# Kernel tuning notes

Measured on AMD Instinct MI355X. Metric: run time of the kernel, lower is better.

The kernel has to match this reference:

```python
import jax, jax.numpy as jnp
import numpy as np

N, E, DIN, DOUT, H = 50000, 800000, 256, 128, 8
DH = DOUT // H  # per-head dim = 16


def setup_inputs() -> dict:
    key = jax.random.key(0)
    k1, k2, k3, k4, k5 = jax.random.split(key, 5)
    x = jax.random.normal(k1, (N, DIN), dtype=jnp.float32)
    edge_index = jax.random.randint(k2, (2, E), 0, N)
    W_trans = jax.random.normal(k3, (DOUT, DIN), dtype=jnp.float32) / np.sqrt(DIN).astype(np.float32)
    W_att = jax.random.normal(k4, (1, 2 * DH), dtype=jnp.float32) / np.sqrt(2 * DH).astype(np.float32)
    b_att = jax.random.normal(k5, (1,), dtype=jnp.float32) * 0.01
    return {"x": x, "W_trans": W_trans, "W_att": W_att, "b_att": b_att, "edge_index": edge_index}


def reference(x, W_trans, W_att, b_att, edge_index):
    n = x.shape[0]
    # append self-loops (as in the torch module)
    loops = jnp.arange(n, dtype=edge_index.dtype)
    ei = jnp.concatenate([edge_index, jnp.stack([loops, loops])], axis=1)  # [2, E+N]
    src, dst = ei[0], ei[1]

    # linear transform, split heads: [n, H, DH]
    h = (x @ W_trans.T).reshape(n, H, DH)
    h_i = h[src]  # [Etot, H, DH]
    h_j = h[dst]  # [Etot, H, DH]

    # per-edge attention score: concat -> linear -> leaky_relu(0.2)
    s = jnp.concatenate([h_i, h_j], axis=-1) @ W_att.T + b_att  # [Etot, H, 1]
    s = jnp.where(s >= 0, s, 0.2 * s)

    # softmax(dim=0)*exp_sum/scatter_add(exp) == exp(s)/segment_sum(exp(s)) per dst node
    e = jnp.exp(s)
    denom = jax.ops.segment_sum(e, dst, num_segments=n)  # [n, H, 1]
    att = e / denom[dst]

    out = jax.ops.segment_sum(h_i * att, dst, num_segments=n)  # [n, H, DH]
    return out.reshape(n, DOUT)  # head_fusion='cat'
```

## Files before the change

### kernel.cpp

```cpp
#include <hip/hip_runtime.h>


constexpr int DIN  = 256;
constexpr int DOUT = 128;
constexpr int H    = 8;
constexpr int BKT  = 128;
constexpr int CAP  = 2560;
constexpr int CHUNK = 2048;
constexpr int MAXNB = 512;

typedef __attribute__((ext_vector_type(8))) short bf16x8;
typedef __attribute__((ext_vector_type(4))) float f32x4;

__device__ __forceinline__ float lrelu(float s) { return s >= 0.0f ? s : 0.2f * s; }

__device__ __forceinline__ unsigned short f2bf(float f) {
  unsigned u = __float_as_uint(f);
  u += 0x7FFF + ((u >> 16) & 1);
  return (unsigned short)(u >> 16);
}
__device__ __forceinline__ float bflo(unsigned u) { return __uint_as_float(u << 16); }
__device__ __forceinline__ float bfhi(unsigned u) { return __uint_as_float(u & 0xFFFF0000u); }

__device__ __forceinline__ int wave_incl_scan(int v, int lane) {
#pragma unroll
  for (int d = 1; d < 64; d <<= 1) {
    int t = __shfl_up(v, d, 64);
    if (lane >= d) v += t;
  }
  return v;
}

__global__ void conv_w(const float* __restrict__ W, unsigned short* __restrict__ Wbf,
                       int n, int* __restrict__ bcount, int nb) {
  int i = blockIdx.x * blockDim.x + threadIdx.x;
  if (i < n) Wbf[i] = f2bf(W[i]);
  if (i < nb) bcount[i] = 0;
}

__global__ __launch_bounds__(256) void bp(const int* __restrict__ ei,
                                          int* __restrict__ bcount,
                                          unsigned* __restrict__ pair_buf,
                                          int E, int nb) {
  __shared__ int hist[MAXNB];
  __shared__ int gbase[MAXNB];
  int c0 = blockIdx.x * CHUNK;
  for (int i = threadIdx.x; i < nb; i += 256) hist[i] = 0;
  __syncthreads();
  int dcache[8];
#pragma unroll
  for (int q = 0; q < 8; ++q) {
    int e = c0 + q * 256 + threadIdx.x;
    dcache[q] = (e < E) ? ei[E + e] : -1;
    if (dcache[q] >= 0) atomicAdd(&hist[dcache[q] >> 7], 1);
  }
  __syncthreads();
  for (int i = threadIdx.x; i < nb; i += 256) {
    int c = hist[i];
    gbase[i] = c ? atomicAdd(&bcount[i], c) : 0;
  }
  __syncthreads();
  for (int i = threadIdx.x; i < nb; i += 256) hist[i] = 0;
  __syncthreads();
  int scache[8];
#pragma unroll
  for (int q = 0; q < 8; ++q) {
    int e = c0 + q * 256 + threadIdx.x;
    scache[q] = (dcache[q] >= 0) ? ei[e] : 0;
  }
#pragma unroll
  for (int q = 0; q < 8; ++q) {
    if (dcache[q] >= 0) {
      int bk = dcache[q] >> 7;
      int r = atomicAdd(&hist[bk], 1);
      pair_buf[bk * CAP + gbase[bk] + r] =
          ((unsigned)scache[q] << 8) | (unsigned)(dcache[q] & 127);
    }
  }
}

__global__ __launch_bounds__(256, 2) void gemm(const float* __restrict__ x,
                                               const unsigned short* __restrict__ Wbf,
                                               unsigned short* __restrict__ hbf,
                                               int N) {
  __shared__ __align__(16) unsigned short Wlds[DOUT * DIN];
  {
    const int tid = threadIdx.x;
#pragma unroll
    for (int i = 0; i < 16; ++i) {
      int c = i * 256 + tid;
      int t = c >> 9, ks = (c >> 6) & 7, L = c & 63;
      const unsigned short* gp = Wbf + ((t * 16 + (L & 15)) * DIN + ks * 32 + (L >> 4) * 8);
      *(bf16x8*)&Wlds[c * 8] = *(const bf16x8*)gp;
    }
  }
  __syncthreads();
  int wid = blockIdx.x * 4 + (threadIdx.x >> 6);
  int m0 = wid * 32;
  if (m0 >= N) return;
  int lane = threadIdx.x & 63;
  int mr = lane & 15, kg = lane >> 4;
  int r0 = m0 + mr;       if (r0 >= N) r0 = N - 1;
  int r1 = m0 + 16 + mr;  if (r1 >= N) r1 = N - 1;
  const float* xr0 = x + (size_t)r0 * DIN + kg * 8;
  const float* xr1 = x + (size_t)r1 * DIN + kg * 8;
  const unsigned short* fb = Wlds + lane * 8;

  f32x4 acc[2][8];
#pragma unroll
  for (int mt = 0; mt < 2; ++mt)
#pragma unroll
    for (int t = 0; t < 8; ++t) acc[mt][t] = (f32x4){0.f, 0.f, 0.f, 0.f};

  float4 p00 = *(const float4*)xr0, p01 = *(const float4*)(xr0 + 4);
  float4 p10 = *(const float4*)xr1, p11 = *(const float4*)(xr1 + 4);
#pragma unroll
  for (int ks = 0; ks < 8; ++ks) {
    bf16x8 a0, a1;
    a0[0] = (short)f2bf(p00.x); a0[1] = (short)f2bf(p00.y);
    a0[2] = (short)f2bf(p00.z); a0[3] = (short)f2bf(p00.w);
    a0[4] = (short)f2bf(p01.x); a0[5] = (short)f2bf(p01.y);
    a0[6] = (short)f2bf(p01.z); a0[7] = (short)f2bf(p01.w);
    a1[0] = (short)f2bf(p10.x); a1[1] = (short)f2bf(p10.y);
    a1[2] = (short)f2bf(p10.z); a1[3] = (short)f2bf(p10.w);
    a1[4] = (short)f2bf(p11.x); a1[5] = (short)f2bf(p11.y);
    a1[6] = (short)f2bf(p11.z); a1[7] = (short)f2bf(p11.w);
    if (ks < 7) {
      p00 = *(const float4*)(xr0 + (ks + 1) * 32);
      p01 = *(const float4*)(xr0 + (ks + 1) * 32 + 4);
      p10 = *(const float4*)(xr1 + (ks + 1) * 32);
      p11 = *(const float4*)(xr1 + (ks + 1) * 32 + 4);
    }
#pragma unroll
    for (int t = 0; t < 8; ++t) {
      bf16x8 b = *(const bf16x8*)(fb + ((t * 8 + ks) << 9));
      acc[0][t] = __builtin_amdgcn_mfma_f32_16x16x32_bf16(a0, b, acc[0][t], 0, 0, 0);
      acc[1][t] = __builtin_amdgcn_mfma_f32_16x16x32_bf16(a1, b, acc[1][t], 0, 0, 0);
    }
  }
#pragma unroll
  for (int mt = 0; mt < 2; ++mt)
#pragma unroll
    for (int t = 0; t < 8; ++t)
#pragma unroll
      for (int r = 0; r < 4; ++r) {
        int row = m0 + mt * 16 + kg * 4 + r;
        if (row < N) hbf[(size_t)row * DOUT + t * 16 + mr] = f2bf(acc[mt][t][r]);
      }
}

__global__ __launch_bounds__(256) void node_scores(const unsigned short* __restrict__ hbf,
                                                   const float* __restrict__ Wa,
                                                   float* __restrict__ a_src,
                                                   float* __restrict__ a_dst,
                                                   int NH) {
  int idx = blockIdx.x * 256 + threadIdx.x;
  if (idx >= NH) return;
  int v = idx >> 3, hh = idx & 7;
  const unsigned short* hp = hbf + (size_t)v * DOUT + hh * 16;
  uint4 p0 = *(const uint4*)hp;
  uint4 p1 = *(const uint4*)(hp + 8);
  float hv[16];
  hv[0] = bflo(p0.x); hv[1] = bfhi(p0.x); hv[2] = bflo(p0.y); hv[3] = bfhi(p0.y);
  hv[4] = bflo(p0.z); hv[5] = bfhi(p0.z); hv[6] = bflo(p0.w); hv[7] = bfhi(p0.w);
  hv[8] = bflo(p1.x); hv[9] = bfhi(p1.x); hv[10] = bflo(p1.y); hv[11] = bfhi(p1.y);
  hv[12] = bflo(p1.z); hv[13] = bfhi(p1.z); hv[14] = bflo(p1.w); hv[15] = bfhi(p1.w);
  float s1 = 0.f, s2 = 0.f;
#pragma unroll
  for (int d = 0; d < 16; ++d) {
    s1 += hv[d] * Wa[d];
    s2 += hv[d] * Wa[16 + d];
  }
  a_src[idx] = s1;
  a_dst[idx] = s2;
}

__global__ __launch_bounds__(512) void agg(const unsigned* __restrict__ pair_buf,
                                           const int* __restrict__ bcount,
                                           const unsigned short* __restrict__ hbf,
                                           const float* __restrict__ a_src,
                                           const float* __restrict__ a_dst,
                                           const float* __restrict__ b_att,
                                           float* __restrict__ out, int N) {
  __shared__ int cnt[BKT];
  __shared__ int off[BKT];
  __shared__ int cur[BKT];
  __shared__ int wsum[2];
  __shared__ unsigned short slist[CAP];
  const int t = threadIdx.x;
  const int B = blockIdx.x;
  const int v0 = B * BKT;
  if (t < BKT) cnt[t] = 0;
  __syncthreads();
  const int cntE = min(bcount[B], CAP);
  const unsigned* reg = pair_buf + (size_t)B * CAP;
  for (int i = t; i < cntE; i += 512) atomicAdd(&cnt[reg[i] & 127], 1);
  __syncthreads();
  int val = 0, inc = 0;
  if (t < BKT) {
    val = cnt[t];
    inc = wave_incl_scan(val, t & 63);
    if ((t & 63) == 63) wsum[t >> 6] = inc;
  }
  __syncthreads();
  if (t < BKT) {
    int ex = inc - val + ((t >= 64) ? wsum[0] : 0);
    off[t] = ex;
    cur[t] = ex;
  }
  __syncthreads();
  for (int i = t; i < cntE; i += 512) {
    unsigned p = reg[i];
    int k = atomicAdd(&cur[p & 127], 1);
    slist[k] = (unsigned short)(p >> 8);
  }
  __syncthreads();
  const float bb = b_att[0];
  const int grp = t >> 4, sl = t & 15, head = sl >> 1;
  for (int nd = grp; nd < BKT; nd += 32) {
    int v = v0 + nd;
    if (v >= N) continue;
    float ad = a_dst[(size_t)v * H + head] + bb;
    int beg = off[nd], end = cur[nd];
    float a0 = 0, a1 = 0, a2 = 0, a3 = 0, a4 = 0, a5 = 0, a6 = 0, a7 = 0, den = 0;
    int sa = (beg < end) ? slist[beg] : 0;
    int sb = (beg + 1 < end) ? slist[beg + 1] : 0;
    for (int j = beg; j < end; j += 2) {
      int sa2 = (j + 2 < end) ? slist[j + 2] : 0;
      int sb2 = (j + 3 < end) ? slist[j + 3] : 0;
      float asa = a_src[(size_t)sa * H + head];
      float asb = a_src[(size_t)sb * H + head];
      uint4 ua = *(const uint4*)(hbf + (size_t)sa * DOUT + sl * 8);
      uint4 ub = *(const uint4*)(hbf + (size_t)sb * DOUT + sl * 8);
      float ea = __expf(lrelu(asa + ad));
      float eb = (j + 1 < end) ? __expf(lrelu(asb + ad)) : 0.f;
      den += ea + eb;
      a0 += ea * bflo(ua.x) + eb * bflo(ub.x);
      a1 += ea * bfhi(ua.x) + eb * bfhi(ub.x);
      a2 += ea * bflo(ua.y) + eb * bflo(ub.y);
      a3 += ea * bfhi(ua.y) + eb * bfhi(ub.y);
      a4 += ea * bflo(ua.z) + eb * bflo(ub.z);
      a5 += ea * bfhi(ua.z) + eb * bfhi(ub.z);
      a6 += ea * bflo(ua.w) + eb * bflo(ub.w);
      a7 += ea * bfhi(ua.w) + eb * bfhi(ub.w);
      sa = sa2; sb = sb2;
    }
    float es = __expf(lrelu(a_src[(size_t)v * H + head] + ad));
    uint4 u = *(const uint4*)(hbf + (size_t)v * DOUT + sl * 8);
    float inv = 1.0f / (den + es);
    float4 o0 = make_float4((a0 + es * bflo(u.x)) * inv, (a1 + es * bfhi(u.x)) * inv,
                            (a2 + es * bflo(u.y)) * inv, (a3 + es * bfhi(u.y)) * inv);
    float4 o1 = make_float4((a4 + es * bflo(u.z)) * inv, (a5 + es * bfhi(u.z)) * inv,
                            (a6 + es * bflo(u.w)) * inv, (a7 + es * bfhi(u.w)) * inv);
    *(float4*)&out[(size_t)v * DOUT + sl * 8] = o0;
    *(float4*)&out[(size_t)v * DOUT + sl * 8 + 4] = o1;
  }
}

extern "C" void kernel_launch(void* const* d_in, const int* in_sizes, int n_in,
                              void* d_out, int out_size, void* d_ws, size_t ws_size,
                              hipStream_t stream) {
  const float* x     = (const float*)d_in[0];
  const float* W     = (const float*)d_in[1];
  const float* Wa    = (const float*)d_in[2];
  const float* b_att = (const float*)d_in[3];
  const int*   ei    = (const int*)d_in[4];
  const int N  = in_sizes[0] / DIN;
  const int E  = in_sizes[4] / 2;
  const int NB = (N + BKT - 1) / BKT;
  float* out = (float*)d_out;

  char* p = (char*)d_ws;
  auto take = [&p](size_t bytes) {
    uintptr_t u = ((uintptr_t)p + 15) & ~(uintptr_t)15;
    p = (char*)(u + bytes);
    return (void*)u;
  };
  unsigned short* hbf = (unsigned short*)take((size_t)N * DOUT * 2);
  unsigned short* Wbf = (unsigned short*)take((size_t)DOUT * DIN * 2);
  float* a_src        = (float*)take((size_t)N * H * 4);
  float* a_dst        = (float*)take((size_t)N * H * 4);
  int* bcount         = (int*)take((size_t)NB * 4);
  unsigned* pair_buf  = (unsigned*)take((size_t)NB * CAP * 4);

  dim3 b256(256);
  const int cw_blocks   = (DOUT * DIN + 255) / 256;
  const int bp_blocks   = (E + CHUNK - 1) / CHUNK;
  const int gemm_blocks = ((N + 31) / 32 + 3) / 4;
  const int ns_blocks   = (N * H + 255) / 256;

  conv_w<<<dim3(cw_blocks), b256, 0, stream>>>(W, Wbf, DOUT * DIN, bcount, NB);
  bp<<<dim3(bp_blocks), b256, 0, stream>>>(ei, bcount, pair_buf, E, NB);
  gemm<<<dim3(gemm_blocks), b256, 0, stream>>>(x, Wbf, hbf, N);
  node_scores<<<dim3(ns_blocks), b256, 0, stream>>>(hbf, Wa, a_src, a_dst, N * H);
  agg<<<dim3(NB), dim3(512), 0, stream>>>(pair_buf, bcount, hbf, a_src, a_dst,
                                          b_att, out, N);
}
```

Before: 176.2 us.

## Store features head-major and split aggregation blocks per head

The transformed features and per-node scores are stored head-major ([H][N][16]). The aggregation grid is split into one block per bucket and head, with 4 lanes per destination node. Each head's gather then touches a compact 1.6 MB slice that fits better in cache, and there are eight times as many blocks for parallelism. In exchange, every block rebuilds the bucket's CSR in shared memory (eight times the pair_buf reads and LDS sorting), gathers shrink to 8-byte loads, and the GEMM writes become more scattered.

```diff
diff --git a/kernel.cpp b/kernel.cpp
--- a/kernel.cpp
+++ b/kernel.cpp
@@ -81,7 +81,7 @@
 
 __global__ __launch_bounds__(256, 2) void gemm(const float* __restrict__ x,
                                                const unsigned short* __restrict__ Wbf,
-                                               unsigned short* __restrict__ hbf,
+                                               unsigned short* __restrict__ hT,
                                                int N) {
   __shared__ __align__(16) unsigned short Wlds[DOUT * DIN];
   {
@@ -145,19 +145,19 @@
 #pragma unroll
       for (int r = 0; r < 4; ++r) {
         int row = m0 + mt * 16 + kg * 4 + r;
-        if (row < N) hbf[(size_t)row * DOUT + t * 16 + mr] = f2bf(acc[mt][t][r]);
+        if (row < N) hT[(size_t)t * N * 16 + (size_t)row * 16 + mr] = f2bf(acc[mt][t][r]);
       }
 }
 
-__global__ __launch_bounds__(256) void node_scores(const unsigned short* __restrict__ hbf,
+__global__ __launch_bounds__(256) void node_scores(const unsigned short* __restrict__ hT,
                                                    const float* __restrict__ Wa,
-                                                   float* __restrict__ a_src,
-                                                   float* __restrict__ a_dst,
-                                                   int NH) {
-  int idx = blockIdx.x * 256 + threadIdx.x;
-  if (idx >= NH) return;
-  int v = idx >> 3, hh = idx & 7;
-  const unsigned short* hp = hbf + (size_t)v * DOUT + hh * 16;
+                                                   float* __restrict__ a_srcT,
+                                                   float* __restrict__ a_dstT,
+                                                   int N) {
+  int v = blockIdx.x * 256 + threadIdx.x;
+  int h = blockIdx.y;
+  if (v >= N) return;
+  const unsigned short* hp = hT + (size_t)h * N * 16 + (size_t)v * 16;
   uint4 p0 = *(const uint4*)hp;
   uint4 p1 = *(const uint4*)(hp + 8);
   float hv[16];
@@ -171,15 +171,15 @@
     s1 += hv[d] * Wa[d];
     s2 += hv[d] * Wa[16 + d];
   }
-  a_src[idx] = s1;
-  a_dst[idx] = s2;
+  a_srcT[(size_t)h * N + v] = s1;
+  a_dstT[(size_t)h * N + v] = s2;
 }
 
 __global__ __launch_bounds__(512) void agg(const unsigned* __restrict__ pair_buf,
                                            const int* __restrict__ bcount,
-                                           const unsigned short* __restrict__ hbf,
-                                           const float* __restrict__ a_src,
-                                           const float* __restrict__ a_dst,
+                                           const unsigned short* __restrict__ hT,
+                                           const float* __restrict__ a_srcT,
+                                           const float* __restrict__ a_dstT,
                                            const float* __restrict__ b_att,
                                            float* __restrict__ out, int N) {
   __shared__ int cnt[BKT];
@@ -188,12 +188,13 @@
   __shared__ int wsum[2];
   __shared__ unsigned short slist[CAP];
   const int t = threadIdx.x;
-  const int B = blockIdx.x;
-  const int v0 = B * BKT;
+  const int bkt = blockIdx.x >> 3;
+  const int head = blockIdx.x & 7;
+  const int v0 = bkt * BKT;
   if (t < BKT) cnt[t] = 0;
   __syncthreads();
-  const int cntE = min(bcount[B], CAP);
-  const unsigned* reg = pair_buf + (size_t)B * CAP;
+  const int cntE = min(bcount[bkt], CAP);
+  const unsigned* reg = pair_buf + (size_t)bkt * CAP;
   for (int i = t; i < cntE; i += 512) atomicAdd(&cnt[reg[i] & 127], 1);
   __syncthreads();
   int val = 0, inc = 0;
@@ -216,45 +217,38 @@
   }
   __syncthreads();
   const float bb = b_att[0];
-  const int grp = t >> 4, sl = t & 15, head = sl >> 1;
-  for (int nd = grp; nd < BKT; nd += 32) {
-    int v = v0 + nd;
-    if (v >= N) continue;
-    float ad = a_dst[(size_t)v * H + head] + bb;
-    int beg = off[nd], end = cur[nd];
-    float a0 = 0, a1 = 0, a2 = 0, a3 = 0, a4 = 0, a5 = 0, a6 = 0, a7 = 0, den = 0;
-    int sa = (beg < end) ? slist[beg] : 0;
-    int sb = (beg + 1 < end) ? slist[beg + 1] : 0;
-    for (int j = beg; j < end; j += 2) {
-      int sa2 = (j + 2 < end) ? slist[j + 2] : 0;
-      int sb2 = (j + 3 < end) ? slist[j + 3] : 0;
-      float asa = a_src[(size_t)sa * H + head];
-      float asb = a_src[(size_t)sb * H + head];
-      uint4 ua = *(const uint4*)(hbf + (size_t)sa * DOUT + sl * 8);
-      uint4 ub = *(const uint4*)(hbf + (size_t)sb * DOUT + sl * 8);
-      float ea = __expf(lrelu(asa + ad));
-      float eb = (j + 1 < end) ? __expf(lrelu(asb + ad)) : 0.f;
-      den += ea + eb;
-      a0 += ea * bflo(ua.x) + eb * bflo(ub.x);
-      a1 += ea * bfhi(ua.x) + eb * bfhi(ub.x);
-      a2 += ea * bflo(ua.y) + eb * bflo(ub.y);
-      a3 += ea * bfhi(ua.y) + eb * bfhi(ub.y);
-      a4 += ea * bflo(ua.z) + eb * bflo(ub.z);
-      a5 += ea * bfhi(ua.z) + eb * bfhi(ub.z);
-      a6 += ea * bflo(ua.w) + eb * bflo(ub.w);
-      a7 += ea * bfhi(ua.w) + eb * bfhi(ub.w);
-      sa = sa2; sb = sb2;
-    }
-    float es = __expf(lrelu(a_src[(size_t)v * H + head] + ad));
-    uint4 u = *(const uint4*)(hbf + (size_t)v * DOUT + sl * 8);
-    float inv = 1.0f / (den + es);
-    float4 o0 = make_float4((a0 + es * bflo(u.x)) * inv, (a1 + es * bfhi(u.x)) * inv,
-                            (a2 + es * bflo(u.y)) * inv, (a3 + es * bfhi(u.y)) * inv);
-    float4 o1 = make_float4((a4 + es * bflo(u.z)) * inv, (a5 + es * bfhi(u.z)) * inv,
-                            (a6 + es * bflo(u.w)) * inv, (a7 + es * bfhi(u.w)) * inv);
-    *(float4*)&out[(size_t)v * DOUT + sl * 8] = o0;
-    *(float4*)&out[(size_t)v * DOUT + sl * 8 + 4] = o1;
-  }
+  const int grp = t >> 2, l = t & 3;
+  int v = v0 + grp;
+  if (v >= N) return;
+  const unsigned short* hTh = hT + (size_t)head * N * 16;
+  const float* asT = a_srcT + (size_t)head * N;
+  float ad = a_dstT[(size_t)head * N + v] + bb;
+  int beg = off[grp], end = cur[grp];
+  float c0 = 0, c1 = 0, c2 = 0, c3 = 0, den = 0;
+  int sa = (beg < end) ? slist[beg] : 0;
+  int sb = (beg + 1 < end) ? slist[beg + 1] : 0;
+  for (int j = beg; j < end; j += 2) {
+    int sa2 = (j + 2 < end) ? slist[j + 2] : 0;
+    int sb2 = (j + 3 < end) ? slist[j + 3] : 0;
+    float asa = asT[sa];
+    float asb = asT[sb];
+    uint2 ua = *(const uint2*)(hTh + (size_t)sa * 16 + l * 4);
+    uint2 ub = *(const uint2*)(hTh + (size_t)sb * 16 + l * 4);
+    float ea = __expf(lrelu(asa + ad));
+    float eb = (j + 1 < end) ? __expf(lrelu(asb + ad)) : 0.f;
+    den += ea + eb;
+    c0 += ea * bflo(ua.x) + eb * bflo(ub.x);
+    c1 += ea * bfhi(ua.x) + eb * bfhi(ub.x);
+    c2 += ea * bflo(ua.y) + eb * bflo(ub.y);
+    c3 += ea * bfhi(ua.y) + eb * bfhi(ub.y);
+    sa = sa2; sb = sb2;
+  }
+  float es = __expf(lrelu(asT[v] + ad));
+  uint2 u = *(const uint2*)(hTh + (size_t)v * 16 + l * 4);
+  float inv = 1.0f / (den + es);
+  float4 o = make_float4((c0 + es * bflo(u.x)) * inv, (c1 + es * bfhi(u.x)) * inv,
+                         (c2 + es * bflo(u.y)) * inv, (c3 + es * bfhi(u.y)) * inv);
+  *(float4*)&out[(size_t)v * DOUT + head * 16 + l * 4] = o;
 }
 
 extern "C" void kernel_launch(void* const* d_in, const int* in_sizes, int n_in,
@@ -276,10 +270,10 @@
     p = (char*)(u + bytes);
     return (void*)u;
   };
-  unsigned short* hbf = (unsigned short*)take((size_t)N * DOUT * 2);
+  unsigned short* hT  = (unsigned short*)take((size_t)N * DOUT * 2);
   unsigned short* Wbf = (unsigned short*)take((size_t)DOUT * DIN * 2);
-  float* a_src        = (float*)take((size_t)N * H * 4);
-  float* a_dst        = (float*)take((size_t)N * H * 4);
+  float* a_srcT       = (float*)take((size_t)N * H * 4);
+  float* a_dstT       = (float*)take((size_t)N * H * 4);
   int* bcount         = (int*)take((size_t)NB * 4);
   unsigned* pair_buf  = (unsigned*)take((size_t)NB * CAP * 4);
 
@@ -287,12 +281,11 @@
   const int cw_blocks   = (DOUT * DIN + 255) / 256;
   const int bp_blocks   = (E + CHUNK - 1) / CHUNK;
   const int gemm_blocks = ((N + 31) / 32 + 3) / 4;
-  const int ns_blocks   = (N * H + 255) / 256;
 
   conv_w<<<dim3(cw_blocks), b256, 0, stream>>>(W, Wbf, DOUT * DIN, bcount, NB);
   bp<<<dim3(bp_blocks), b256, 0, stream>>>(ei, bcount, pair_buf, E, NB);
-  gemm<<<dim3(gemm_blocks), b256, 0, stream>>>(x, Wbf, hbf, N);
-  node_scores<<<dim3(ns_blocks), b256, 0, stream>>>(hbf, Wa, a_src, a_dst, N * H);
-  agg<<<dim3(NB), dim3(512), 0, stream>>>(pair_buf, bcount, hbf, a_src, a_dst,
-                                          b_att, out, N);
-}
+  gemm<<<dim3(gemm_blocks), b256, 0, stream>>>(x, Wbf, hT, N);
+  node_scores<<<dim3((N + 255) / 256, H), b256, 0, stream>>>(hT, Wa, a_srcT, a_dstT, N);
+  agg<<<dim3(NB * H), dim3(512), 0, stream>>>(pair_buf, bcount, hT, a_srcT, a_dstT,
+                                              b_att, out, N);
+}
```

Result: slower. 197.1 us (+11.9%).
